# Performance work log

Hardware: AMD Instinct MI355X
Metric: run time of the kernel (lower is better)

## Reference

```python
import jax, jax.numpy as jnp
import numpy as np

TAU = 2.0      # LIFNode default tau
V_TH = 1.0     # default v_threshold
ALPHA = 4.0    # surrogate.Sigmoid default alpha

@jax.custom_vjp
def spike_fn(x):
    # heaviside: spike if membrane potential crosses threshold
    return (x >= 0.0).astype(x.dtype)

def _spike_fwd(x):
    return spike_fn(x), x

def _spike_bwd(x, g):
    s = jax.nn.sigmoid(ALPHA * x)
    return (g * ALPHA * s * (1.0 - s),)

spike_fn.defvjp(_spike_fwd, _spike_bwd)

def lif_step(v, inp):
    # decay_input=True, v_reset=0.0 (hard reset):
    # v <- v + (inp - v)/tau ; spike = H(v - v_th) ; v <- v*(1-spike)
    v = v + (inp - v) / TAU
    s = spike_fn(v - V_TH)
    v = v * (1.0 - s)
    return v, s

def setup_inputs() -> dict:
    key = jax.random.key(0)
    k_x, k1, k2, k3 = jax.random.split(key, 4)
    T, B, H, W = 16, 64, 150, 400
    x = jax.random.normal(k_x, (T, B, H, W), dtype=jnp.float32)
    # torch Linear default init: U(-1/sqrt(fan_in), 1/sqrt(fan_in))
    def lin_init(k, out_f, in_f):
        bound = 1.0 / np.sqrt(in_f)
        return jax.random.uniform(k, (out_f, in_f), dtype=jnp.float32,
                                  minval=-bound, maxval=bound)
    W1 = lin_init(k1, 200, 60000)
    W2 = lin_init(k2, 50, 200)
    W3 = lin_init(k3, 2, 50)
    return {"x": x, "W1": W1, "W2": W2, "W3": W3}

def reference(x, W1, W2, W3):
    T, B = x.shape[0], x.shape[1]
    xf = x.reshape(T, B, -1)  # layer.Flatten over non-(T,B) dims -> [T,B,60000]
    D1, D2, D3 = W1.shape[0], W2.shape[0], W3.shape[0]

    def step(carry, xt):
        v1, v2, v3 = carry
        h1 = xt @ W1.T            # [B,200]
        v1, s1 = lif_step(v1, h1)
        h2 = s1 @ W2.T            # [B,50]
        v2, s2 = lif_step(v2, h2)
        h3 = s2 @ W3.T            # [B,2]
        v3, s3 = lif_step(v3, h3)
        return (v1, v2, v3), s3

    init = (jnp.zeros((B, D1), x.dtype),
            jnp.zeros((B, D2), x.dtype),
            jnp.zeros((B, D3), x.dtype))
    _, out = jax.lax.scan(step, init, xf)  # out: [T,B,2] spike trains
    return out
```

## Files before the change

### kernel.cpp

```cpp
#include <hip/hip_runtime.h>
#include <hip/hip_bf16.h>

#define T_STEPS 16
#define BATCH   64
#define M_ROWS  1024
#define K_DIM   60000
#define N1      200
#define N2      50
#define N3      2
#define NPAD    256
#define HN      (M_ROWS * N1)
#define BK      32

typedef __attribute__((ext_vector_type(8)))  short bf16x8;
typedef __attribute__((ext_vector_type(16))) float f32x16;

static __device__ __forceinline__ bf16x8 cvt8(float4 lo, float4 hi) {
    union { bf16x8 v; __hip_bfloat162 h[4]; } u;
    u.h[0] = __float22bfloat162_rn(make_float2(lo.x, lo.y));
    u.h[1] = __float22bfloat162_rn(make_float2(lo.z, lo.w));
    u.h[2] = __float22bfloat162_rn(make_float2(hi.x, hi.y));
    u.h[3] = __float22bfloat162_rn(make_float2(hi.z, hi.w));
    return u.v;
}

static __device__ __forceinline__ float bf2f(unsigned short u) {
    unsigned int x = (unsigned int)u << 16;
    return __uint_as_float(x);
}

typedef __attribute__((address_space(3))) unsigned int       lds_u32;
typedef __attribute__((address_space(1))) const unsigned int glb_u32;
static __device__ __forceinline__ void gll16(const void* g, void* l) {
    __builtin_amdgcn_global_load_lds((glb_u32*)(unsigned long long)g,
                                     (lds_u32*)(unsigned int)(unsigned long long)l,
                                     16, 0, 0);
}

__global__ __launch_bounds__(256)
void cvt_w1(const float* __restrict__ w1, unsigned short* __restrict__ w1b) {
    const size_t e = ((size_t)blockIdx.x * 256 + threadIdx.x) * 8;
    if (e >= (size_t)N1 * K_DIM) return;
    *(bf16x8*)(w1b + e) = cvt8(*(const float4*)(w1 + e),
                               *(const float4*)(w1 + e + 4));
}

template <int KSEG, int KSTEPS, int NWG>
__global__ __launch_bounds__(512, 4)
void gemm_lds(const float* __restrict__ x,
              const unsigned short* __restrict__ w1b,
              unsigned short* __restrict__ part) {
    __shared__ __align__(16) char smem[2][24576];

    const int tid = threadIdx.x;
    const int l   = tid & 63;
    const int wv  = tid >> 6;
    const int wm  = wv & 1;
    const int wn  = wv >> 1;

    const int hw      = blockIdx.y * 8 + blockIdx.x;
    const int logical = (hw & 7) * (NWG / 8) + (hw >> 3);
    const int s  = logical >> 3;
    const int mt = logical & 7;

    const int m0 = mt * 128;
    const int k0 = s * KSEG;

    const int ar = tid >> 2;
    const int ag = tid & 3;
    const float* asrc = x + (size_t)(m0 + ar) * K_DIM + k0 + ag * 8;
    const int aw_off = ar * 64 + ((ag ^ ((ar >> 1) & 3)) << 4);

    const char* bsrc[2];
    int bl_off[2];
    #pragma unroll
    for (int j = 0; j < 2; ++j) {
        const int c   = wv * 2 + j;
        const int row = c * 16 + (l >> 2);
        bl_off[j] = 8192 + c * 1024 + l * 16;
        bsrc[j]   = (const char*)(w1b + (size_t)row * K_DIM + k0)
                    + (((l & 3) ^ ((row >> 1) & 3)) << 4);
    }

    f32x16 acc[2][2];
    #pragma unroll
    for (int i = 0; i < 2; ++i)
        #pragma unroll
        for (int j = 0; j < 2; ++j)
            #pragma unroll
            for (int q = 0; q < 16; ++q) acc[i][j][q] = 0.f;

    float4 pA[2][2];
    gll16(bsrc[0], smem[0] + bl_off[0]);
    gll16(bsrc[1], smem[0] + bl_off[1]);
    pA[0][0] = *(const float4*)asrc;
    pA[0][1] = *(const float4*)(asrc + 4);
    pA[1][0] = *(const float4*)(asrc + BK);
    pA[1][1] = *(const float4*)(asrc + BK + 4);
    *(bf16x8*)(smem[0] + aw_off) = cvt8(pA[0][0], pA[0][1]);
    __builtin_amdgcn_sched_barrier(0);
    asm volatile("s_waitcnt vmcnt(2)" ::: "memory");
    __syncthreads();

    const int fr = l & 31;
    const int fh = (l >> 5) * 16;

    #pragma unroll 2
    for (int it = 0; it < KSTEPS; ++it) {
        const int cur = it & 1;
        const bool more = (it + 1) < KSTEPS;

        if (more) {
            gll16(bsrc[0] + (size_t)(it + 1) * (BK * 2), smem[cur ^ 1] + bl_off[0]);
            gll16(bsrc[1] + (size_t)(it + 1) * (BK * 2), smem[cur ^ 1] + bl_off[1]);
            const int jn = (it + 2 < KSTEPS) ? (it + 2) : (KSTEPS - 1);
            pA[cur][0] = *(const float4*)(asrc + jn * BK);
            pA[cur][1] = *(const float4*)(asrc + jn * BK + 4);
        }
        __builtin_amdgcn_sched_barrier(0);

        const char* ab = smem[cur];
        const char* bb = smem[cur] + 8192;
        #pragma unroll
        for (int kk = 0; kk < 2; ++kk) {
            const int r0 = wm * 64 + fr;
            const int r1 = wm * 64 + 32 + fr;
            bf16x8 a0 = *(const bf16x8*)(ab + r0 * 64 + ((kk * 32 + fh) ^ (((r0 >> 1) & 3) << 4)));
            bf16x8 a1 = *(const bf16x8*)(ab + r1 * 64 + ((kk * 32 + fh) ^ (((r1 >> 1) & 3) << 4)));
            #pragma unroll
            for (int fn = 0; fn < 2; ++fn) {
                const int n = wn * 64 + fn * 32 + fr;
                bf16x8 bv = *(const bf16x8*)(bb + n * 64 + ((kk * 32 + fh) ^ (((n >> 1) & 3) << 4)));
                acc[0][fn] = __builtin_amdgcn_mfma_f32_32x32x16_bf16(a0, bv, acc[0][fn], 0, 0, 0);
                acc[1][fn] = __builtin_amdgcn_mfma_f32_32x32x16_bf16(a1, bv, acc[1][fn], 0, 0, 0);
            }
        }

        if (more) {
            *(bf16x8*)(smem[cur ^ 1] + aw_off) = cvt8(pA[cur ^ 1][0], pA[cur ^ 1][1]);
            __builtin_amdgcn_sched_barrier(0);
            asm volatile("s_waitcnt vmcnt(2)" ::: "memory");
            __syncthreads();
        }
    }

    const int col = l & 31;
    const int rhi = (l >> 5) * 4;
    #pragma unroll
    for (int fm = 0; fm < 2; ++fm)
        #pragma unroll
        for (int fn = 0; fn < 2; ++fn) {
            const int gn = wn * 64 + fn * 32 + col;
            if (gn < N1) {
                const int gmb = m0 + wm * 64 + fm * 32 + rhi;
                #pragma unroll
                for (int r = 0; r < 16; ++r) {
                    const int gm = gmb + (r & 3) + 8 * (r >> 2);
                    __hip_bfloat16 hv = __float2bfloat16(acc[fm][fn][r]);
                    part[(size_t)s * HN + (size_t)gm * N1 + gn] = *(unsigned short*)&hv;
                }
            }
        }
}

template <int KSPLIT>
__global__ __launch_bounds__(256)
void reduce_kernel(const unsigned short* __restrict__ part, float* __restrict__ h1) {
    const size_t f = ((size_t)blockIdx.x * 256 + threadIdx.x) * 2;
    float a0 = 0.f, a1 = 0.f;
    #pragma unroll 25
    for (int s = 0; s < KSPLIT; ++s) {
        const unsigned int v = *(const unsigned int*)(part + (size_t)s * HN + f);
        a0 += bf2f((unsigned short)(v & 0xFFFFu));
        a1 += bf2f((unsigned short)(v >> 16));
    }
    h1[f]     = a0;
    h1[f + 1] = a1;
}

__global__ __launch_bounds__(256)
void tail_kernel(const float* __restrict__ h1,
                 const float* __restrict__ w2, const float* __restrict__ w3,
                 float* __restrict__ out) {
    __shared__ float w2s[N2 * N1];
    __shared__ float w3s[N3 * N2];
    __shared__ unsigned long long msk[T_STEPS][4];

    const int b    = blockIdx.x;
    const int i    = threadIdx.x;
    const int wv   = i >> 6;
    const int lane = i & 63;

    for (int o = i; o < (N2 * N1) / 4; o += 256)
        ((float4*)w2s)[o] = ((const float4*)w2)[o];
    if (i < N3 * N2) w3s[i] = w3[i];

    float h[T_STEPS];
    #pragma unroll
    for (int t = 0; t < T_STEPS; ++t)
        h[t] = (i < N1) ? h1[(size_t)(t * BATCH + b) * N1 + i] : 0.f;

    float v1 = 0.f;
    #pragma unroll
    for (int t = 0; t < T_STEPS; ++t) {
        v1 += (h[t] - v1) * 0.5f;
        bool sp = (v1 - 1.0f) >= 0.f;
        unsigned long long m = __ballot(sp);
        if (sp) v1 = 0.f;
        if (lane == 0) msk[t][wv] = m;
    }
    __syncthreads();

    if (wv == 0) {
        float v2 = 0.f, v3 = 0.f;
        for (int t = 0; t < T_STEPS; ++t) {
            float h2 = 0.f;
            if (lane < N2) {
                #pragma unroll
                for (int w = 0; w < 4; ++w) {
                    unsigned long long m = msk[t][w];
                    while (m) {
                        int lz = __builtin_ctzll(m);
                        m &= m - 1;
                        h2 += w2s[lane * N1 + (w * 64 + lz)];
                    }
                }
            }
            v2 += (h2 - v2) * 0.5f;
            bool sp2 = (v2 - 1.0f) >= 0.f;
            unsigned long long bal2 = __ballot(sp2);
            if (sp2) v2 = 0.f;

            float h3 = 0.f;
            if (lane < N3) {
                unsigned long long m = bal2;
                while (m) {
                    int j = __builtin_ctzll(m);
                    m &= m - 1;
                    h3 += w3s[lane * N2 + j];
                }
            }
            v3 += (h3 - v3) * 0.5f;
            bool sp3 = (v3 - 1.0f) >= 0.f;
            if (lane < N3)
                out[(size_t)(t * BATCH + b) * N3 + lane] = sp3 ? 1.f : 0.f;
            if (sp3) v3 = 0.f;
        }
    }
}

extern "C" void kernel_launch(void* const* d_in, const int* in_sizes, int n_in,
                              void* d_out, int out_size, void* d_ws, size_t ws_size,
                              hipStream_t stream) {
    const float* x  = (const float*)d_in[0];
    const float* w1 = (const float*)d_in[1];
    const float* w2 = (const float*)d_in[2];
    const float* w3 = (const float*)d_in[3];
    float* out = (float*)d_out;

    const size_t w1b_bytes = (size_t)NPAD * K_DIM * 2;
    const size_t h1_bytes  = (size_t)HN * 4;
    const size_t need125 = (size_t)125 * HN * 2 + h1_bytes + w1b_bytes;
    const bool big = ws_size >= need125;

    const int ksplit = big ? 125 : 25;
    unsigned short* part = (unsigned short*)d_ws;
    float* h1 = (float*)((char*)d_ws + (size_t)ksplit * HN * 2);
    unsigned short* w1b = (unsigned short*)((char*)h1 + h1_bytes);

    cvt_w1<<<(N1 * K_DIM / 8 + 255) / 256, 256, 0, stream>>>(w1, w1b);
    if (big) {
        dim3 g(8, 125);
        gemm_lds<480, 15, 1000><<<g, 512, 0, stream>>>(x, w1b, part);
        reduce_kernel<125><<<HN / 512, 256, 0, stream>>>(part, h1);
    } else {
        dim3 g(8, 25);
        gemm_lds<2400, 75, 200><<<g, 512, 0, stream>>>(x, w1b, part);
        reduce_kernel<25><<<HN / 512, 256, 0, stream>>>(part, h1);
    }
    tail_kernel<<<BATCH, 256, 0, stream>>>(h1, w2, w3, out);
}
```

Measured before the change: 120.9 us.

## Fuse W1 fp32-to-bf16 conversion into GEMM B-tile loads

Drops the separate cvt_w1 pre-pass and its bf16 workspace copy of W1. The GEMM now loads fp32 W1 through registers, converts it to bf16 and writes it to LDS, the same way A is handled. The direct global-to-LDS async loads are gone, and the K loop is fully unrolled. Each of the 8 M-tile workgroups now re-reads fp32 W1, which doubles those bytes versus bf16. This also adds register pressure and conversion work inside the GEMM, in exchange for removing a launch and a full pass over W1.

```diff
diff --git a/kernel.cpp b/kernel.cpp
--- a/kernel.cpp
+++ b/kernel.cpp
@@ -8,7 +8,6 @@
 #define N1      200
 #define N2      50
 #define N3      2
-#define NPAD    256
 #define HN      (M_ROWS * N1)
 #define BK      32
 
@@ -29,26 +28,10 @@
     return __uint_as_float(x);
 }
 
-typedef __attribute__((address_space(3))) unsigned int       lds_u32;
-typedef __attribute__((address_space(1))) const unsigned int glb_u32;
-static __device__ __forceinline__ void gll16(const void* g, void* l) {
-    __builtin_amdgcn_global_load_lds((glb_u32*)(unsigned long long)g,
-                                     (lds_u32*)(unsigned int)(unsigned long long)l,
-                                     16, 0, 0);
-}
-
-__global__ __launch_bounds__(256)
-void cvt_w1(const float* __restrict__ w1, unsigned short* __restrict__ w1b) {
-    const size_t e = ((size_t)blockIdx.x * 256 + threadIdx.x) * 8;
-    if (e >= (size_t)N1 * K_DIM) return;
-    *(bf16x8*)(w1b + e) = cvt8(*(const float4*)(w1 + e),
-                               *(const float4*)(w1 + e + 4));
-}
-
 template <int KSEG, int KSTEPS, int NWG>
 __global__ __launch_bounds__(512, 4)
 void gemm_lds(const float* __restrict__ x,
-              const unsigned short* __restrict__ w1b,
+              const float* __restrict__ w1,
               unsigned short* __restrict__ part) {
     __shared__ __align__(16) char smem[2][24576];
 
@@ -71,16 +54,13 @@
     const float* asrc = x + (size_t)(m0 + ar) * K_DIM + k0 + ag * 8;
     const int aw_off = ar * 64 + ((ag ^ ((ar >> 1) & 3)) << 4);
 
-    const char* bsrc[2];
-    int bl_off[2];
-    #pragma unroll
-    for (int j = 0; j < 2; ++j) {
-        const int c   = wv * 2 + j;
-        const int row = c * 16 + (l >> 2);
-        bl_off[j] = 8192 + c * 1024 + l * 16;
-        bsrc[j]   = (const char*)(w1b + (size_t)row * K_DIM + k0)
-                    + (((l & 3) ^ ((row >> 1) & 3)) << 4);
-    }
+    const int br = tid >> 1;
+    const int bh = tid & 1;
+    const bool bvalid = br < N1;
+    const float* bsrc = w1 + (size_t)br * K_DIM + k0 + bh * 16;
+    const int bg0 = bh * 2;
+    const int bw_off0 = 8192 + br * 64 + (((bg0)     ^ ((br >> 1) & 3)) << 4);
+    const int bw_off1 = 8192 + br * 64 + (((bg0 + 1) ^ ((br >> 1) & 3)) << 4);
 
     f32x16 acc[2][2];
     #pragma unroll
@@ -91,28 +71,41 @@
             for (int q = 0; q < 16; ++q) acc[i][j][q] = 0.f;
 
     float4 pA[2][2];
-    gll16(bsrc[0], smem[0] + bl_off[0]);
-    gll16(bsrc[1], smem[0] + bl_off[1]);
+    float4 pB[4];
+    #pragma unroll
+    for (int j = 0; j < 4; ++j) pB[j] = (float4){0.f, 0.f, 0.f, 0.f};
+
     pA[0][0] = *(const float4*)asrc;
     pA[0][1] = *(const float4*)(asrc + 4);
+    if (bvalid) {
+        pB[0] = *(const float4*)bsrc;
+        pB[1] = *(const float4*)(bsrc + 4);
+        pB[2] = *(const float4*)(bsrc + 8);
+        pB[3] = *(const float4*)(bsrc + 12);
+    }
     pA[1][0] = *(const float4*)(asrc + BK);
     pA[1][1] = *(const float4*)(asrc + BK + 4);
     *(bf16x8*)(smem[0] + aw_off) = cvt8(pA[0][0], pA[0][1]);
-    __builtin_amdgcn_sched_barrier(0);
-    asm volatile("s_waitcnt vmcnt(2)" ::: "memory");
+    *(bf16x8*)(smem[0] + bw_off0) = cvt8(pB[0], pB[1]);
+    *(bf16x8*)(smem[0] + bw_off1) = cvt8(pB[2], pB[3]);
     __syncthreads();
 
     const int fr = l & 31;
     const int fh = (l >> 5) * 16;
 
-    #pragma unroll 2
+    #pragma unroll
     for (int it = 0; it < KSTEPS; ++it) {
         const int cur = it & 1;
         const bool more = (it + 1) < KSTEPS;
 
         if (more) {
-            gll16(bsrc[0] + (size_t)(it + 1) * (BK * 2), smem[cur ^ 1] + bl_off[0]);
-            gll16(bsrc[1] + (size_t)(it + 1) * (BK * 2), smem[cur ^ 1] + bl_off[1]);
+            if (bvalid) {
+                const float* bp = bsrc + (size_t)(it + 1) * BK;
+                pB[0] = *(const float4*)bp;
+                pB[1] = *(const float4*)(bp + 4);
+                pB[2] = *(const float4*)(bp + 8);
+                pB[3] = *(const float4*)(bp + 12);
+            }
             const int jn = (it + 2 < KSTEPS) ? (it + 2) : (KSTEPS - 1);
             pA[cur][0] = *(const float4*)(asrc + jn * BK);
             pA[cur][1] = *(const float4*)(asrc + jn * BK + 4);
@@ -137,9 +130,11 @@
         }
 
         if (more) {
-            *(bf16x8*)(smem[cur ^ 1] + aw_off) = cvt8(pA[cur ^ 1][0], pA[cur ^ 1][1]);
+            char* nb = smem[cur ^ 1];
+            *(bf16x8*)(nb + aw_off)  = cvt8(pA[cur ^ 1][0], pA[cur ^ 1][1]);
+            *(bf16x8*)(nb + bw_off0) = cvt8(pB[0], pB[1]);
+            *(bf16x8*)(nb + bw_off1) = cvt8(pB[2], pB[3]);
             __builtin_amdgcn_sched_barrier(0);
-            asm volatile("s_waitcnt vmcnt(2)" ::: "memory");
             __syncthreads();
         }
     }
@@ -258,24 +253,21 @@
     const float* w3 = (const float*)d_in[3];
     float* out = (float*)d_out;
 
-    const size_t w1b_bytes = (size_t)NPAD * K_DIM * 2;
     const size_t h1_bytes  = (size_t)HN * 4;
-    const size_t need125 = (size_t)125 * HN * 2 + h1_bytes + w1b_bytes;
+    const size_t need125 = (size_t)125 * HN * 2 + h1_bytes;
     const bool big = ws_size >= need125;
 
     const int ksplit = big ? 125 : 25;
     unsigned short* part = (unsigned short*)d_ws;
     float* h1 = (float*)((char*)d_ws + (size_t)ksplit * HN * 2);
-    unsigned short* w1b = (unsigned short*)((char*)h1 + h1_bytes);
-
-    cvt_w1<<<(N1 * K_DIM / 8 + 255) / 256, 256, 0, stream>>>(w1, w1b);
+
     if (big) {
         dim3 g(8, 125);
-        gemm_lds<480, 15, 1000><<<g, 512, 0, stream>>>(x, w1b, part);
+        gemm_lds<480, 15, 1000><<<g, 512, 0, stream>>>(x, w1, part);
         reduce_kernel<125><<<HN / 512, 256, 0, stream>>>(part, h1);
     } else {
         dim3 g(8, 25);
-        gemm_lds<2400, 75, 200><<<g, 512, 0, stream>>>(x, w1b, part);
+        gemm_lds<2400, 75, 200><<<g, 512, 0, stream>>>(x, w1, part);
         reduce_kernel<25><<<HN / 512, 256, 0, stream>>>(part, h1);
     }
     tail_kernel<<<BATCH, 256, 0, stream>>>(h1, w2, w3, out);
```

Result: faster. 102.0 us (-15.6%).
